# Performance work log

Measured on AMD Instinct MI355X. Metric: run time of the kernel, lower is better.

Reference implementation:

```python
import jax, jax.numpy as jnp
import numpy as np

DIM = 256
STATE = 128
RANK = 64
BATCH = 16
H = 64
W = 64
BLOCK = 64
LN_EPS = 1e-5


def _linear(z, w, b):
    # torch nn.Linear: z @ w.T + b, w: [out, in]
    return jnp.matmul(z, w.T) + b


def _depthwise_conv1d(y, conv_w, conv_b):
    # y: [B, L, D] -> torch Conv1d(D, D, k=7, pad=3, groups=D)
    lhs = jnp.transpose(y, (0, 2, 1))  # [B, D, L]
    out = jax.lax.conv_general_dilated(
        lhs, conv_w, window_strides=(1,), padding=[(3, 3)],
        feature_group_count=STATE,
        dimension_numbers=("NCH", "OIH", "NCH"))
    out = out + conv_b[None, :, None]
    return jnp.transpose(out, (0, 2, 1))  # [B, L, D]


def _scan_parallel(seq, in_proj_w, in_proj_b, U, V, B_w, B_b, out_w, out_b,
                   conv_w, conv_b):
    # seq: [B, L, C]; L > PARALLEL_THRESHOLD path of the torch module
    Bn, L, _ = seq.shape
    x = _linear(seq, in_proj_w, in_proj_b)   # [B, L, D]
    bx = _linear(x, B_w, B_b)                # [B, L, D]
    n_blocks = (L + BLOCK - 1) // BLOCK
    pad_len = n_blocks * BLOCK - L
    if pad_len > 0:
        bx = jnp.pad(bx, ((0, 0), (0, pad_len), (0, 0)))
    # [B, n_blocks, BLOCK, D] -> scan over time axis BLOCK
    bx_blocks = bx.reshape(Bn, n_blocks, BLOCK, STATE)
    bx_t = jnp.transpose(bx_blocks, (2, 0, 1, 3))  # [BLOCK, B, n_blocks, D]

    def step(h, xt):
        # h: [B, n_blocks, D]; low-rank transition h @ V @ U^T + Bx
        h = jnp.matmul(jnp.matmul(h, V), U.T) + xt
        return h, h

    h0 = jnp.zeros((Bn, n_blocks, STATE), dtype=seq.dtype)
    _, ys = jax.lax.scan(step, h0, bx_t)           # [BLOCK, B, n_blocks, D]
    y_flat = jnp.transpose(ys, (1, 2, 0, 3)).reshape(Bn, n_blocks * BLOCK, STATE)
    y_flat = y_flat + _depthwise_conv1d(y_flat, conv_w, conv_b)
    if pad_len > 0:
        y_flat = y_flat[:, :L, :]
    return _linear(y_flat, out_w, out_b)           # [B, L, C]


def _layer_norm(z, g, b):
    mu = jnp.mean(z, axis=-1, keepdims=True)
    var = jnp.var(z, axis=-1, keepdims=True)
    return (z - mu) * jax.lax.rsqrt(var + LN_EPS) * g + b


def setup_inputs() -> dict:
    key = jax.random.key(0)
    ks = jax.random.split(key, 16)
    s = 0.02
    return {
        "x": jax.random.normal(ks[0], (BATCH, DIM, H, W), dtype=jnp.float32),
        "in_proj_w": jax.random.normal(ks[1], (STATE, DIM)) * s,
        "in_proj_b": jnp.zeros((STATE,), jnp.float32),
        "U": jax.random.normal(ks[2], (STATE, RANK)) * s,
        "V": jax.random.normal(ks[3], (STATE, RANK)) * s,
        "B_w": jax.random.normal(ks[4], (STATE, STATE)) * s,
        "B_b": jnp.zeros((STATE,), jnp.float32),
        "out_w": jax.random.normal(ks[5], (DIM, STATE)) * s,
        "out_b": jnp.zeros((DIM,), jnp.float32),
        "gate_w": jax.random.normal(ks[6], (DIM, DIM)) * s,
        "gate_b": jnp.zeros((DIM,), jnp.float32),
        "norm_g": jnp.ones((DIM,), jnp.float32),
        "norm_b": jnp.zeros((DIM,), jnp.float32),
        "conv_w": jax.random.normal(ks[7], (STATE, 1, 7)) * s,
        "conv_b": jnp.zeros((STATE,), jnp.float32),
    }


def reference(x, in_proj_w, in_proj_b, U, V, B_w, B_b, out_w, out_b,
              gate_w, gate_b, norm_g, norm_b, conv_w, conv_b):
    Bn, C, h, w = x.shape
    seq_lr = jnp.transpose(x, (0, 2, 3, 1)).reshape(Bn, h * w, C)
    seq_rl = seq_lr[:, ::-1, :]
    scan = lambda s: _scan_parallel(s, in_proj_w, in_proj_b, U, V, B_w, B_b,
                                    out_w, out_b, conv_w, conv_b)
    y_lr = scan(seq_lr)
    y_rl = scan(seq_rl)[:, ::-1, :]
    y = 0.5 * (y_lr + y_rl)
    gate = jax.nn.sigmoid(_linear(seq_lr, gate_w, gate_b))
    y = gate * y
    y = _layer_norm(y + seq_lr, norm_g, norm_b)
    y = jnp.transpose(y.reshape(Bn, h, w, C), (0, 3, 1, 2))
    state_seq = _linear(seq_lr, in_proj_w, in_proj_b)
    return y, state_seq
```

## Files before the change

### kernel.cpp

```cpp
#include <hip/hip_runtime.h>
#include <hip/hip_bf16.h>

#define DIMC 256
#define STATE 128
#define RANK 64
#define NBATCH 16
#define LSEQ 4096
#define NROWS (NBATCH*LSEQ)
#define LN_EPS 1e-5f
#define XSTR 264
#define X1STR 136

typedef __attribute__((ext_vector_type(8))) short frag8;
typedef __attribute__((ext_vector_type(4))) float f32x4;

union Pack4 { __hip_bfloat16 h[4]; uint2 u; };
union Pack8 { __hip_bfloat16 h[8]; uint4 u; };

__device__ inline void gload_lds16(const void* g, void* l) {
    __builtin_amdgcn_global_load_lds((const __attribute__((address_space(1))) void*)g,
                                     (__attribute__((address_space(3))) void*)l, 16, 0, 0);
}

template<int NROWSW, int NTHR>
__device__ inline void stage_wslice(const __hip_bfloat16* __restrict__ W, int Krow, int k0,
                                    __hip_bfloat16* dst, int t) {
    constexpr int ROUNDS = (NROWSW*64) / (NTHR*16);
    const int lane = t & 63, w = t >> 6;
    #pragma unroll
    for (int j = 0; j < ROUNDS; ++j) {
        int base = (w*ROUNDS + j) << 10;
        int X = base + lane*16;
        int r = X >> 6;
        int cg = (X >> 4) & 3;
        const __hip_bfloat16* src = W + (size_t)r*Krow + k0 + ((cg ^ ((r>>1)&3)) << 3);
        gload_lds16(src, (char*)dst + base);
    }
}
__device__ inline frag8 ld_wfrag(const __hip_bfloat16* buf, int row, int q) {
    return *(const frag8*)((const char*)buf + (row<<6) + ((q ^ ((row>>1)&3))<<4));
}

__global__ __launch_bounds__(128) void a_kernel(const float* __restrict__ U, const float* __restrict__ V,
                                                __hip_bfloat16* __restrict__ At) {
    int i = blockIdx.x, j = threadIdx.x;
    float s = 0.f;
    #pragma unroll
    for (int r = 0; r < RANK; ++r) s += V[i*RANK + r] * U[j*RANK + r];
    At[j*STATE + i] = __float2bfloat16(s);
}

__global__ __launch_bounds__(256) void prep_weights(const float* __restrict__ in_w, const float* __restrict__ B_w,
                                                    const float* __restrict__ gate_w, const float* __restrict__ out_w,
                                                    __hip_bfloat16* __restrict__ in_wb, __hip_bfloat16* __restrict__ B_wb,
                                                    __hip_bfloat16* __restrict__ gate_wb, __hip_bfloat16* __restrict__ out_wb) {
    int idx = blockIdx.x*256 + threadIdx.x;
    int which = blockIdx.y;
    if (which == 0) { if (idx < STATE*DIMC)  in_wb[idx]   = __float2bfloat16(in_w[idx]); }
    else if (which == 1) { if (idx < STATE*STATE) B_wb[idx] = __float2bfloat16(B_w[idx]); }
    else if (which == 2) { if (idx < DIMC*DIMC)  gate_wb[idx] = __float2bfloat16(gate_w[idx]); }
    else { if (idx < DIMC*STATE) out_wb[idx] = __float2bfloat16(out_w[idx]); }
}

template<int NTHR>
__device__ inline void stage_x64(const float* __restrict__ xb, int l0,
                                 __hip_bfloat16* __restrict__ xs, int t) {
    constexpr int UN = 1024 / NTHR;
    #pragma unroll
    for (int uu = 0; uu < UN; ++uu) {
        int unit = t + uu*NTHR;
        int lg = unit & 15, cg = unit >> 4;
        int l = lg*4;
        float4 v0 = *(const float4*)(xb + (size_t)(cg*4+0)*LSEQ + l0 + l);
        float4 v1 = *(const float4*)(xb + (size_t)(cg*4+1)*LSEQ + l0 + l);
        float4 v2 = *(const float4*)(xb + (size_t)(cg*4+2)*LSEQ + l0 + l);
        float4 v3 = *(const float4*)(xb + (size_t)(cg*4+3)*LSEQ + l0 + l);
        const float* p0 = (const float*)&v0; const float* p1 = (const float*)&v1;
        const float* p2 = (const float*)&v2; const float* p3 = (const float*)&v3;
        #pragma unroll
        for (int li = 0; li < 4; ++li) {
            Pack4 p;
            p.h[0] = __float2bfloat16(p0[li]);
            p.h[1] = __float2bfloat16(p1[li]);
            p.h[2] = __float2bfloat16(p2[li]);
            p.h[3] = __float2bfloat16(p3[li]);
            int row = l + li;
            int col = (cg*4) ^ ((row&3)<<3);
            *(uint2*)(xs + (size_t)row*XSTR + col) = p.u;
        }
    }
}
__device__ inline frag8 ld_xfrag(const __hip_bfloat16* __restrict__ xs, int row, int k) {
    return *(const frag8*)(xs + (size_t)row*XSTR + (k ^ ((row&3)<<3)));
}

__global__ __launch_bounds__(512) void gemm_inB(const float* __restrict__ x,
                                                const __hip_bfloat16* __restrict__ in_wb, const float* __restrict__ in_b,
                                                const __hip_bfloat16* __restrict__ B_wb, const float* __restrict__ B_b,
                                                float* __restrict__ state_out, float* __restrict__ bx) {
    __shared__ __hip_bfloat16 xs[64*XSTR];
    __shared__ __hip_bfloat16 wsl[2][4096];
    __hip_bfloat16* x1s = xs;
    const int t = threadIdx.x;
    const int lane = t & 63;
    const int c = lane & 15, q = lane >> 4;
    const int w = t >> 6, wm = w >> 1, wc = w & 1;
    const int r0 = blockIdx.x * 64;
    const int b = r0 >> 12, l0 = r0 & 4095;

    stage_x64<512>(x + (size_t)b*DIMC*LSEQ, l0, xs, t);
    stage_wslice<STATE,512>(in_wb, DIMC, 0, wsl[0], t);
    __syncthreads();

    f32x4 acc[4] = {};
    #pragma unroll
    for (int i = 0; i < 8; ++i) {
        if (i < 7) stage_wslice<STATE,512>(in_wb, DIMC, (i+1)*32, wsl[(i+1)&1], t);
        frag8 af = ld_xfrag(xs, wm*16 + c, i*32 + q*8);
        #pragma unroll
        for (int nt = 0; nt < 4; ++nt) {
            frag8 bf = ld_wfrag(wsl[i&1], wc*64 + nt*16 + c, q);
            acc[nt] = __builtin_amdgcn_mfma_f32_16x16x32_bf16(af, bf, acc[nt], 0, 0, 0);
        }
        __syncthreads();
    }

    stage_wslice<STATE,512>(B_wb, STATE, 0, wsl[0], t);

    #pragma unroll
    for (int nt = 0; nt < 4; ++nt) {
        int col = wc*64 + nt*16 + c;
        float bb = in_b[col];
        #pragma unroll
        for (int r = 0; r < 4; ++r) {
            int row = wm*16 + q*4 + r;
            float v = acc[nt][r] + bb;
            state_out[(size_t)(r0 + row)*STATE + col] = v;
            x1s[(size_t)row*X1STR + (col ^ ((row&3)<<3))] = __float2bfloat16(v);
        }
    }
    __syncthreads();

    f32x4 acc2[4] = {};
    #pragma unroll
    for (int i = 0; i < 4; ++i) {
        if (i < 3) stage_wslice<STATE,512>(B_wb, STATE, (i+1)*32, wsl[(i+1)&1], t);
        int row = wm*16 + c;
        frag8 af = *(const frag8*)(x1s + (size_t)row*X1STR + (((i*32) + q*8) ^ ((row&3)<<3)));
        #pragma unroll
        for (int nt = 0; nt < 4; ++nt) {
            frag8 bf = ld_wfrag(wsl[i&1], wc*64 + nt*16 + c, q);
            acc2[nt] = __builtin_amdgcn_mfma_f32_16x16x32_bf16(af, bf, acc2[nt], 0, 0, 0);
        }
        __syncthreads();
    }
    const int orow = r0 + wm*16 + q*4;
    #pragma unroll
    for (int nt = 0; nt < 4; ++nt) {
        int col = wc*64 + nt*16 + c;
        float bb = B_b[col];
        #pragma unroll
        for (int r = 0; r < 4; ++r)
            bx[(size_t)(orow + r)*STATE + col] = acc2[nt][r] + bb;
    }
}

#define HSTRIDE 144
__global__ __launch_bounds__(256, 1) void scan_mfma(const float* __restrict__ bx,
                                                    const __hip_bfloat16* __restrict__ At,
                                                    __hip_bfloat16* __restrict__ ylr,
                                                    __hip_bfloat16* __restrict__ yrl) {
    __shared__ __hip_bfloat16 Hb[16 * HSTRIDE];
    const int t = threadIdx.x;
    const int l = t & 63;
    const int wm = t >> 6;
    const int c = l & 15;
    const int q = l >> 4;

    const int S   = blockIdx.x * 16 + c;
    const int dir = S >> 10;
    const int b   = (S >> 6) & 15;
    const int blk = S & 63;
    const int lp0 = blk * 64;
    const int lorig0 = dir ? (LSEQ - 1 - lp0) : lp0;
    const int sgnstep = dir ? -STATE : STATE;

    const float* bxrow = bx + ((size_t)b*LSEQ + lorig0)*STATE;
    __hip_bfloat16* yrow = (dir ? yrl : ylr) + ((size_t)b*LSEQ + lp0)*STATE;

    frag8 afr[2][4];
    #pragma unroll
    for (int mm = 0; mm < 2; ++mm)
        #pragma unroll
        for (int kc = 0; kc < 4; ++kc)
            afr[mm][kc] = *(const frag8*)(At + (size_t)((wm*2+mm)*16 + c)*STATE + kc*32 + q*8);

    for (int k = t; k < 16*HSTRIDE; k += 256) Hb[k] = __float2bfloat16(0.f);
    __syncthreads();

    f32x4 pf[2];
    #pragma unroll
    for (int mm = 0; mm < 2; ++mm)
        pf[mm] = *(const f32x4*)(bxrow + (wm*2+mm)*16 + q*4);

    for (int tt = 0; tt < 64; ++tt) {
        frag8 bfr[4];
        #pragma unroll
        for (int kc = 0; kc < 4; ++kc)
            bfr[kc] = *(const frag8*)(&Hb[c*HSTRIDE + kc*32 + q*8]);

        f32x4 acc[2];
        #pragma unroll
        for (int mm = 0; mm < 2; ++mm) {
            f32x4 a = {0.f, 0.f, 0.f, 0.f};
            #pragma unroll
            for (int kc = 0; kc < 4; ++kc)
                a = __builtin_amdgcn_mfma_f32_16x16x32_bf16(afr[mm][kc], bfr[kc], a, 0, 0, 0);
            acc[mm] = a + pf[mm];
        }
        if (tt < 63) {
            bxrow += sgnstep;
            #pragma unroll
            for (int mm = 0; mm < 2; ++mm)
                pf[mm] = *(const f32x4*)(bxrow + (wm*2+mm)*16 + q*4);
        }

        Pack4 pk[2];
        #pragma unroll
        for (int mm = 0; mm < 2; ++mm) {
            pk[mm].h[0] = __float2bfloat16(acc[mm][0]);
            pk[mm].h[1] = __float2bfloat16(acc[mm][1]);
            pk[mm].h[2] = __float2bfloat16(acc[mm][2]);
            pk[mm].h[3] = __float2bfloat16(acc[mm][3]);
        }
        #pragma unroll
        for (int mm = 0; mm < 2; ++mm)
            *(uint2*)(yrow + (wm*2+mm)*16 + q*4) = pk[mm].u;
        yrow += STATE;

        __syncthreads();
        #pragma unroll
        for (int mm = 0; mm < 2; ++mm)
            *(uint2*)(&Hb[c*HSTRIDE + (wm*2+mm)*16 + q*4]) = pk[mm].u;
        __syncthreads();
    }
}

__global__ __launch_bounds__(128) void conv_combine(const __hip_bfloat16* __restrict__ ylr,
                                                    const __hip_bfloat16* __restrict__ yrl,
                                                    const float* __restrict__ conv_w, const float* __restrict__ conv_b,
                                                    __hip_bfloat16* __restrict__ u) {
    const int t = threadIdx.x;
    const int s8 = (t & 15) * 8;
    const int l = blockIdx.x * 8 + (t >> 4);
    const int b = blockIdx.y;

    float wv[8][7];
    #pragma unroll
    for (int j = 0; j < 8; ++j)
        #pragma unroll
        for (int i = 0; i < 7; ++i) wv[j][i] = conv_w[(s8+j)*7 + i];

    const __hip_bfloat16* plr = ylr + (size_t)b*LSEQ*STATE;
    const __hip_bfloat16* prl = yrl + (size_t)b*LSEQ*STATE;

    float acc[8];
    {
        Pack8 v; v.u = *(const uint4*)(plr + (size_t)l*STATE + s8);
        #pragma unroll
        for (int j = 0; j < 8; ++j) acc[j] = __bfloat162float(v.h[j]);
    }
    #pragma unroll
    for (int i = 0; i < 7; ++i) {
        int qq = l - 3 + i;
        if (qq >= 0 && qq < LSEQ) {
            Pack8 v; v.u = *(const uint4*)(plr + (size_t)qq*STATE + s8);
            #pragma unroll
            for (int j = 0; j < 8; ++j) acc[j] += wv[j][i] * __bfloat162float(v.h[j]);
        }
    }
    const int lp = LSEQ - 1 - l;
    {
        Pack8 v; v.u = *(const uint4*)(prl + (size_t)lp*STATE + s8);
        #pragma unroll
        for (int j = 0; j < 8; ++j) acc[j] += __bfloat162float(v.h[j]);
    }
    #pragma unroll
    for (int i = 0; i < 7; ++i) {
        int qq = lp - 3 + i;
        if (qq >= 0 && qq < LSEQ) {
            Pack8 v; v.u = *(const uint4*)(prl + (size_t)qq*STATE + s8);
            #pragma unroll
            for (int j = 0; j < 8; ++j) acc[j] += wv[j][i] * __bfloat162float(v.h[j]);
        }
    }
    Pack8 o;
    #pragma unroll
    for (int j = 0; j < 8; ++j) o.h[j] = __float2bfloat16(0.5f*acc[j] + conv_b[s8+j]);
    *(uint4*)(u + ((size_t)b*LSEQ + l)*STATE + s8) = o.u;
}

__global__ __launch_bounds__(512) void fused_out(const float* __restrict__ x, const __hip_bfloat16* __restrict__ ub,
    const __hip_bfloat16* __restrict__ out_wb, const float* __restrict__ out_b,
    const __hip_bfloat16* __restrict__ gate_wb, const float* __restrict__ gate_b,
    const float* __restrict__ norm_g, const float* __restrict__ norm_b,
    float* __restrict__ y) {
    __shared__ __hip_bfloat16 xs[64*XSTR];
    __shared__ __hip_bfloat16 wsl[2][8192];
    __shared__ float lnbuf[4][2][16][2];
    const int t = threadIdx.x;
    const int lane = t & 63, c = lane & 15, q = lane >> 4;
    const int w = t >> 6, wm = w >> 1, wc = w & 1;
    const int r0 = blockIdx.x * 64;
    const int b = r0 >> 12, l0 = r0 & 4095;

    stage_x64<512>(x + (size_t)b*DIMC*LSEQ, l0, xs, t);
    frag8 ufr[4];
    {
        const int arow = r0 + wm*16 + c;
        #pragma unroll
        for (int kc = 0; kc < 4; ++kc)
            ufr[kc] = *(const frag8*)(ub + (size_t)arow*STATE + kc*32 + q*8);
    }
    stage_wslice<DIMC,512>(gate_wb, DIMC, 0, wsl[0], t);
    __syncthreads();

    f32x4 accg[8] = {};
    f32x4 acco[8] = {};
    #pragma unroll
    for (int i = 0; i < 12; ++i) {
        if (i < 11) {
            if (i < 7) stage_wslice<DIMC,512>(gate_wb, DIMC, (i+1)*32, wsl[(i+1)&1], t);
            else       stage_wslice<DIMC,512>(out_wb,  STATE, (i-7)*32, wsl[(i+1)&1], t);
        }
        if (i < 8) {
            frag8 af = ld_xfrag(xs, wm*16 + c, i*32 + q*8);
            #pragma unroll
            for (int nt = 0; nt < 8; ++nt) {
                frag8 bf = ld_wfrag(wsl[i&1], wc*128 + nt*16 + c, q);
                accg[nt] = __builtin_amdgcn_mfma_f32_16x16x32_bf16(af, bf, accg[nt], 0, 0, 0);
            }
        } else {
            frag8 af = ufr[i-8];
            #pragma unroll
            for (int nt = 0; nt < 8; ++nt) {
                frag8 bf = ld_wfrag(wsl[i&1], wc*128 + nt*16 + c, q);
                acco[nt] = __builtin_amdgcn_mfma_f32_16x16x32_bf16(af, bf, acco[nt], 0, 0, 0);
            }
        }
        __syncthreads();
    }

    float s1[4] = {0.f,0.f,0.f,0.f}, s2[4] = {0.f,0.f,0.f,0.f};
    #pragma unroll
    for (int nt = 0; nt < 8; ++nt) {
        int col = wc*128 + nt*16 + c;
        float gb = gate_b[col], ob = out_b[col];
        #pragma unroll
        for (int r = 0; r < 4; ++r) {
            int row = wm*16 + q*4 + r;
            float res = __bfloat162float(xs[(size_t)row*XSTR + (col ^ ((row&3)<<3))]);
            float g = 1.f/(1.f + expf(-(accg[nt][r] + gb)));
            float v = g*(acco[nt][r] + ob) + res;
            accg[nt][r] = v;
            s1[r] += v; s2[r] += v*v;
        }
    }
    #pragma unroll
    for (int m = 1; m <= 8; m <<= 1) {
        #pragma unroll
        for (int r = 0; r < 4; ++r) {
            s1[r] += __shfl_xor(s1[r], m);
            s2[r] += __shfl_xor(s2[r], m);
        }
    }
    if (c == 0) {
        #pragma unroll
        for (int r = 0; r < 4; ++r) {
            lnbuf[wm][wc][q*4 + r][0] = s1[r];
            lnbuf[wm][wc][q*4 + r][1] = s2[r];
        }
    }
    __syncthreads();
    float mu[4], rstd[4];
    #pragma unroll
    for (int r = 0; r < 4; ++r) {
        int row16 = q*4 + r;
        float t1 = lnbuf[wm][0][row16][0] + lnbuf[wm][1][row16][0];
        float t2 = lnbuf[wm][0][row16][1] + lnbuf[wm][1][row16][1];
        float m_ = t1 * (1.f/256.f);
        mu[r] = m_;
        rstd[r] = rsqrtf(t2 * (1.f/256.f) - m_*m_ + LN_EPS);
    }
    #pragma unroll
    for (int nt = 0; nt < 8; ++nt) {
        int col = wc*128 + nt*16 + c;
        float g = norm_g[col], be = norm_b[col];
        float4 v4;
        v4.x = (accg[nt][0] - mu[0]) * rstd[0] * g + be;
        v4.y = (accg[nt][1] - mu[1]) * rstd[1] * g + be;
        v4.z = (accg[nt][2] - mu[2]) * rstd[2] * g + be;
        v4.w = (accg[nt][3] - mu[3]) * rstd[3] * g + be;
        *(float4*)(y + ((size_t)b*DIMC + col)*LSEQ + l0 + wm*16 + q*4) = v4;
    }
}

extern "C" void kernel_launch(void* const* d_in, const int* in_sizes, int n_in,
                              void* d_out, int out_size, void* d_ws, size_t ws_size,
                              hipStream_t stream) {
    const float* x      = (const float*)d_in[0];
    const float* in_w   = (const float*)d_in[1];
    const float* in_b   = (const float*)d_in[2];
    const float* U      = (const float*)d_in[3];
    const float* V      = (const float*)d_in[4];
    const float* B_w    = (const float*)d_in[5];
    const float* B_b    = (const float*)d_in[6];
    const float* out_w  = (const float*)d_in[7];
    const float* out_b  = (const float*)d_in[8];
    const float* gate_w = (const float*)d_in[9];
    const float* gate_b = (const float*)d_in[10];
    const float* norm_g = (const float*)d_in[11];
    const float* norm_b = (const float*)d_in[12];
    const float* conv_w = (const float*)d_in[13];
    const float* conv_b = (const float*)d_in[14];

    float* yfinal = (float*)d_out;
    float* state_out = yfinal + (size_t)NBATCH*DIMC*LSEQ;

    float* ws  = (float*)d_ws;
    float* bxu = ws;
    __hip_bfloat16* ub = (__hip_bfloat16*)ws;
    __hip_bfloat16* Atb16  = (__hip_bfloat16*)(ws + (size_t)NROWS*STATE);
    __hip_bfloat16* in_wb  = Atb16 + STATE*STATE;
    __hip_bfloat16* B_wb   = in_wb + STATE*DIMC;
    __hip_bfloat16* gate_wb= B_wb + STATE*STATE;
    __hip_bfloat16* out_wb = gate_wb + DIMC*DIMC;

    __hip_bfloat16* ylr = (__hip_bfloat16*)yfinal;
    __hip_bfloat16* yrl = ylr + (size_t)NROWS*STATE;

    a_kernel<<<dim3(STATE), dim3(STATE), 0, stream>>>(U, V, Atb16);
    prep_weights<<<dim3(256, 4), dim3(256), 0, stream>>>(in_w, B_w, gate_w, out_w,
                                                         in_wb, B_wb, gate_wb, out_wb);
    gemm_inB<<<dim3(NROWS/64), dim3(512), 0, stream>>>(x, in_wb, in_b, B_wb, B_b, state_out, bxu);
    scan_mfma<<<dim3(128), dim3(256), 0, stream>>>(bxu, Atb16, ylr, yrl);
    conv_combine<<<dim3(LSEQ/8, NBATCH), dim3(128), 0, stream>>>(ylr, yrl, conv_w, conv_b, ub);
    fused_out<<<dim3(NROWS/64), dim3(512), 0, stream>>>(x, ub, out_wb, out_b, gate_wb, gate_b,
                                                        norm_g, norm_b, yfinal);
    (void)in_sizes; (void)n_in; (void)out_size; (void)ws_size;
}
```

Measured before the change: 150.8 us.

## Store bx in bf16 and pipeline weight staging with explicit waitcnt barriers

The intermediate bx tensor is now written in bf16 instead of fp32, which halves its write traffic in gemm_inB and its read traffic in the serial scan kernel. The __syncthreads calls in the GEMM loops are replaced with manual s_waitcnt vmcnt/lgkmcnt plus s_barrier sequences, so the async LDS loads for the next weight slice stay in flight across the barrier. The B_w slice prefetch is folded into the last in_proj iteration, and the state_out store is deferred to the end. The risks are lower bx precision feeding the recurrence and correctness depending on hand-tuned vmcnt counts.

Result: slower. 168.8 us (+12.0%).

```diff
diff --git a/kernel.cpp b/kernel.cpp
--- a/kernel.cpp
+++ b/kernel.cpp
@@ -10,6 +10,10 @@
 #define LN_EPS 1e-5f
 #define XSTR 264
 #define X1STR 136
+
+#define SBAR() asm volatile("s_barrier" ::: "memory")
+#define SCHED_FENCE() __builtin_amdgcn_sched_barrier(0)
+#define LGKM0() asm volatile("s_waitcnt lgkmcnt(0)" ::: "memory")
 
 typedef __attribute__((ext_vector_type(8))) short frag8;
 typedef __attribute__((ext_vector_type(4))) float f32x4;
@@ -97,7 +101,7 @@
 __global__ __launch_bounds__(512) void gemm_inB(const float* __restrict__ x,
                                                 const __hip_bfloat16* __restrict__ in_wb, const float* __restrict__ in_b,
                                                 const __hip_bfloat16* __restrict__ B_wb, const float* __restrict__ B_b,
-                                                float* __restrict__ state_out, float* __restrict__ bx) {
+                                                float* __restrict__ state_out, __hip_bfloat16* __restrict__ bxb) {
     __shared__ __hip_bfloat16 xs[64*XSTR];
     __shared__ __hip_bfloat16 wsl[2][4096];
     __hip_bfloat16* x1s = xs;
@@ -115,18 +119,27 @@
     f32x4 acc[4] = {};
     #pragma unroll
     for (int i = 0; i < 8; ++i) {
-        if (i < 7) stage_wslice<STATE,512>(in_wb, DIMC, (i+1)*32, wsl[(i+1)&1], t);
+        LGKM0();
+        SCHED_FENCE();
+        SBAR();
+        if (i < 7) {
+            stage_wslice<STATE,512>(in_wb, DIMC, (i+1)*32, wsl[(i+1)&1], t);
+        } else {
+            stage_wslice<STATE,512>(B_wb, STATE, 0, wsl[0], t);
+        }
+        asm volatile("s_waitcnt vmcnt(1)" ::: "memory");
+        SBAR();
         frag8 af = ld_xfrag(xs, wm*16 + c, i*32 + q*8);
         #pragma unroll
         for (int nt = 0; nt < 4; ++nt) {
             frag8 bf = ld_wfrag(wsl[i&1], wc*64 + nt*16 + c, q);
             acc[nt] = __builtin_amdgcn_mfma_f32_16x16x32_bf16(af, bf, acc[nt], 0, 0, 0);
         }
-        __syncthreads();
-    }
-
-    stage_wslice<STATE,512>(B_wb, STATE, 0, wsl[0], t);
-
+    }
+
+    LGKM0();
+    SCHED_FENCE();
+    SBAR();
     #pragma unroll
     for (int nt = 0; nt < 4; ++nt) {
         int col = wc*64 + nt*16 + c;
@@ -134,17 +147,26 @@
         #pragma unroll
         for (int r = 0; r < 4; ++r) {
             int row = wm*16 + q*4 + r;
-            float v = acc[nt][r] + bb;
-            state_out[(size_t)(r0 + row)*STATE + col] = v;
-            x1s[(size_t)row*X1STR + (col ^ ((row&3)<<3))] = __float2bfloat16(v);
-        }
-    }
-    __syncthreads();
+            x1s[(size_t)row*X1STR + (col ^ ((row&3)<<3))] = __float2bfloat16(acc[nt][r] + bb);
+        }
+    }
+    LGKM0();
+    SCHED_FENCE();
+    SBAR();
 
     f32x4 acc2[4] = {};
     #pragma unroll
     for (int i = 0; i < 4; ++i) {
-        if (i < 3) stage_wslice<STATE,512>(B_wb, STATE, (i+1)*32, wsl[(i+1)&1], t);
+        LGKM0();
+        SCHED_FENCE();
+        SBAR();
+        if (i < 3) {
+            stage_wslice<STATE,512>(B_wb, STATE, (i+1)*32, wsl[(i+1)&1], t);
+            asm volatile("s_waitcnt vmcnt(1)" ::: "memory");
+        } else {
+            asm volatile("s_waitcnt vmcnt(0)" ::: "memory");
+        }
+        SBAR();
         int row = wm*16 + c;
         frag8 af = *(const frag8*)(x1s + (size_t)row*X1STR + (((i*32) + q*8) ^ ((row&3)<<3)));
         #pragma unroll
@@ -152,21 +174,23 @@
             frag8 bf = ld_wfrag(wsl[i&1], wc*64 + nt*16 + c, q);
             acc2[nt] = __builtin_amdgcn_mfma_f32_16x16x32_bf16(af, bf, acc2[nt], 0, 0, 0);
         }
-        __syncthreads();
-    }
+    }
+
     const int orow = r0 + wm*16 + q*4;
     #pragma unroll
     for (int nt = 0; nt < 4; ++nt) {
         int col = wc*64 + nt*16 + c;
-        float bb = B_b[col];
-        #pragma unroll
-        for (int r = 0; r < 4; ++r)
-            bx[(size_t)(orow + r)*STATE + col] = acc2[nt][r] + bb;
+        float bi = in_b[col], bb = B_b[col];
+        #pragma unroll
+        for (int r = 0; r < 4; ++r) {
+            state_out[(size_t)(orow + r)*STATE + col] = acc[nt][r] + bi;
+            bxb[(size_t)(orow + r)*STATE + col] = __float2bfloat16(acc2[nt][r] + bb);
+        }
     }
 }
 
 #define HSTRIDE 144
-__global__ __launch_bounds__(256, 1) void scan_mfma(const float* __restrict__ bx,
+__global__ __launch_bounds__(256, 1) void scan_mfma(const __hip_bfloat16* __restrict__ bxb,
                                                     const __hip_bfloat16* __restrict__ At,
                                                     __hip_bfloat16* __restrict__ ylr,
                                                     __hip_bfloat16* __restrict__ yrl) {
@@ -185,7 +209,7 @@
     const int lorig0 = dir ? (LSEQ - 1 - lp0) : lp0;
     const int sgnstep = dir ? -STATE : STATE;
 
-    const float* bxrow = bx + ((size_t)b*LSEQ + lorig0)*STATE;
+    const __hip_bfloat16* bxrow = bxb + ((size_t)b*LSEQ + lorig0)*STATE;
     __hip_bfloat16* yrow = (dir ? yrl : ylr) + ((size_t)b*LSEQ + lp0)*STATE;
 
     frag8 afr[2][4];
@@ -198,10 +222,10 @@
     for (int k = t; k < 16*HSTRIDE; k += 256) Hb[k] = __float2bfloat16(0.f);
     __syncthreads();
 
-    f32x4 pf[2];
+    uint2 pf[2];
     #pragma unroll
     for (int mm = 0; mm < 2; ++mm)
-        pf[mm] = *(const f32x4*)(bxrow + (wm*2+mm)*16 + q*4);
+        pf[mm] = *(const uint2*)(bxrow + (wm*2+mm)*16 + q*4);
 
     for (int tt = 0; tt < 64; ++tt) {
         frag8 bfr[4];
@@ -216,13 +240,17 @@
             #pragma unroll
             for (int kc = 0; kc < 4; ++kc)
                 a = __builtin_amdgcn_mfma_f32_16x16x32_bf16(afr[mm][kc], bfr[kc], a, 0, 0, 0);
-            acc[mm] = a + pf[mm];
+            Pack4 pp; pp.u = pf[mm];
+            acc[mm][0] = a[0] + __bfloat162float(pp.h[0]);
+            acc[mm][1] = a[1] + __bfloat162float(pp.h[1]);
+            acc[mm][2] = a[2] + __bfloat162float(pp.h[2]);
+            acc[mm][3] = a[3] + __bfloat162float(pp.h[3]);
         }
         if (tt < 63) {
             bxrow += sgnstep;
             #pragma unroll
             for (int mm = 0; mm < 2; ++mm)
-                pf[mm] = *(const f32x4*)(bxrow + (wm*2+mm)*16 + q*4);
+                pf[mm] = *(const uint2*)(bxrow + (wm*2+mm)*16 + q*4);
         }
 
         Pack4 pk[2];
@@ -329,10 +357,17 @@
     f32x4 acco[8] = {};
     #pragma unroll
     for (int i = 0; i < 12; ++i) {
+        LGKM0();
+        SCHED_FENCE();
+        SBAR();
         if (i < 11) {
             if (i < 7) stage_wslice<DIMC,512>(gate_wb, DIMC, (i+1)*32, wsl[(i+1)&1], t);
             else       stage_wslice<DIMC,512>(out_wb,  STATE, (i-7)*32, wsl[(i+1)&1], t);
-        }
+            asm volatile("s_waitcnt vmcnt(2)" ::: "memory");
+        } else {
+            asm volatile("s_waitcnt vmcnt(0)" ::: "memory");
+        }
+        SBAR();
         if (i < 8) {
             frag8 af = ld_xfrag(xs, wm*16 + c, i*32 + q*8);
             #pragma unroll
@@ -348,8 +383,10 @@
                 acco[nt] = __builtin_amdgcn_mfma_f32_16x16x32_bf16(af, bf, acco[nt], 0, 0, 0);
             }
         }
-        __syncthreads();
-    }
+    }
+    LGKM0();
+    SCHED_FENCE();
+    __syncthreads();
 
     float s1[4] = {0.f,0.f,0.f,0.f}, s2[4] = {0.f,0.f,0.f,0.f};
     #pragma unroll
@@ -428,8 +465,8 @@
     float* state_out = yfinal + (size_t)NBATCH*DIMC*LSEQ;
 
     float* ws  = (float*)d_ws;
-    float* bxu = ws;
-    __hip_bfloat16* ub = (__hip_bfloat16*)ws;
+    __hip_bfloat16* bxb = (__hip_bfloat16*)ws;
+    __hip_bfloat16* ub  = (__hip_bfloat16*)ws;
     __hip_bfloat16* Atb16  = (__hip_bfloat16*)(ws + (size_t)NROWS*STATE);
     __hip_bfloat16* in_wb  = Atb16 + STATE*STATE;
     __hip_bfloat16* B_wb   = in_wb + STATE*DIMC;
@@ -442,8 +479,8 @@
     a_kernel<<<dim3(STATE), dim3(STATE), 0, stream>>>(U, V, Atb16);
     prep_weights<<<dim3(256, 4), dim3(256), 0, stream>>>(in_w, B_w, gate_w, out_w,
                                                          in_wb, B_wb, gate_wb, out_wb);
-    gemm_inB<<<dim3(NROWS/64), dim3(512), 0, stream>>>(x, in_wb, in_b, B_wb, B_b, state_out, bxu);
-    scan_mfma<<<dim3(128), dim3(256), 0, stream>>>(bxu, Atb16, ylr, yrl);
+    gemm_inB<<<dim3(NROWS/64), dim3(512), 0, stream>>>(x, in_wb, in_b, B_wb, B_b, state_out, bxb);
+    scan_mfma<<<dim3(128), dim3(256), 0, stream>>>(bxb, Atb16, ylr, yrl);
     conv_combine<<<dim3(LSEQ/8, NBATCH), dim3(128), 0, stream>>>(ylr, yrl, conv_w, conv_b, ub);
     fused_out<<<dim3(NROWS/64), dim3(512), 0, stream>>>(x, ub, out_wb, out_b, gate_wb, gate_b,
                                                         norm_g, norm_b, yfinal);
```

## Store bx in bf16 and reuse transposed bf16 x in output kernel

Applied to the files above, without the earlier changes.

gemm_inB now writes the transposed, bf16-converted x tile to a workspace buffer. fused_out loads that buffer straight into LDS with global_load_lds instead of re-reading and transposing the fp32 NCHW input. The bx intermediate is also stored as bf16 instead of fp32, which halves scan input traffic. The LDS swizzle widens from row&3 to row&7. The aim is less global memory traffic, at the cost of an extra bf16 x write, bf16 rounding of bx before the recurrence, and reliance on the workspace having room for x_bt.

After: 170.4 us. 13.0% more time.

```diff
diff --git a/kernel.cpp b/kernel.cpp
--- a/kernel.cpp
+++ b/kernel.cpp
@@ -85,19 +85,23 @@
             p.h[2] = __float2bfloat16(p2[li]);
             p.h[3] = __float2bfloat16(p3[li]);
             int row = l + li;
-            int col = (cg*4) ^ ((row&3)<<3);
+            int col = (cg*4) ^ ((row&7)<<3);
             *(uint2*)(xs + (size_t)row*XSTR + col) = p.u;
         }
     }
 }
 __device__ inline frag8 ld_xfrag(const __hip_bfloat16* __restrict__ xs, int row, int k) {
-    return *(const frag8*)(xs + (size_t)row*XSTR + (k ^ ((row&3)<<3)));
+    return *(const frag8*)(xs + (size_t)row*XSTR + (k ^ ((row&7)<<3)));
+}
+__device__ inline frag8 ld_xfrag2(const __hip_bfloat16* __restrict__ xs, int row, int k) {
+    return *(const frag8*)(xs + (size_t)row*DIMC + (k ^ ((row&7)<<3)));
 }
 
 __global__ __launch_bounds__(512) void gemm_inB(const float* __restrict__ x,
                                                 const __hip_bfloat16* __restrict__ in_wb, const float* __restrict__ in_b,
                                                 const __hip_bfloat16* __restrict__ B_wb, const float* __restrict__ B_b,
-                                                float* __restrict__ state_out, float* __restrict__ bx) {
+                                                float* __restrict__ state_out, __hip_bfloat16* __restrict__ bxb,
+                                                __hip_bfloat16* __restrict__ x_bt) {
     __shared__ __hip_bfloat16 xs[64*XSTR];
     __shared__ __hip_bfloat16 wsl[2][4096];
     __hip_bfloat16* x1s = xs;
@@ -112,6 +116,15 @@
     stage_wslice<STATE,512>(in_wb, DIMC, 0, wsl[0], t);
     __syncthreads();
 
+    {
+        int row = t >> 3, sub = t & 7;
+        const char* srcb = (const char*)xs + (size_t)row*(XSTR*2) + sub*64;
+        __hip_bfloat16* dstp = x_bt + (size_t)(r0 + row)*DIMC + sub*32;
+        #pragma unroll
+        for (int j = 0; j < 4; ++j)
+            *(uint4*)(dstp + j*8) = *(const uint4*)(srcb + j*16);
+    }
+
     f32x4 acc[4] = {};
     #pragma unroll
     for (int i = 0; i < 8; ++i) {
@@ -161,12 +174,12 @@
         float bb = B_b[col];
         #pragma unroll
         for (int r = 0; r < 4; ++r)
-            bx[(size_t)(orow + r)*STATE + col] = acc2[nt][r] + bb;
+            bxb[(size_t)(orow + r)*STATE + col] = __float2bfloat16(acc2[nt][r] + bb);
     }
 }
 
 #define HSTRIDE 144
-__global__ __launch_bounds__(256, 1) void scan_mfma(const float* __restrict__ bx,
+__global__ __launch_bounds__(256, 1) void scan_mfma(const __hip_bfloat16* __restrict__ bxb,
                                                     const __hip_bfloat16* __restrict__ At,
                                                     __hip_bfloat16* __restrict__ ylr,
                                                     __hip_bfloat16* __restrict__ yrl) {
@@ -185,7 +198,7 @@
     const int lorig0 = dir ? (LSEQ - 1 - lp0) : lp0;
     const int sgnstep = dir ? -STATE : STATE;
 
-    const float* bxrow = bx + ((size_t)b*LSEQ + lorig0)*STATE;
+    const __hip_bfloat16* bxrow = bxb + ((size_t)b*LSEQ + lorig0)*STATE;
     __hip_bfloat16* yrow = (dir ? yrl : ylr) + ((size_t)b*LSEQ + lp0)*STATE;
 
     frag8 afr[2][4];
@@ -198,10 +211,10 @@
     for (int k = t; k < 16*HSTRIDE; k += 256) Hb[k] = __float2bfloat16(0.f);
     __syncthreads();
 
-    f32x4 pf[2];
+    uint2 pf[2];
     #pragma unroll
     for (int mm = 0; mm < 2; ++mm)
-        pf[mm] = *(const f32x4*)(bxrow + (wm*2+mm)*16 + q*4);
+        pf[mm] = *(const uint2*)(bxrow + (wm*2+mm)*16 + q*4);
 
     for (int tt = 0; tt < 64; ++tt) {
         frag8 bfr[4];
@@ -216,13 +229,17 @@
             #pragma unroll
             for (int kc = 0; kc < 4; ++kc)
                 a = __builtin_amdgcn_mfma_f32_16x16x32_bf16(afr[mm][kc], bfr[kc], a, 0, 0, 0);
-            acc[mm] = a + pf[mm];
+            Pack4 pp; pp.u = pf[mm];
+            acc[mm][0] = a[0] + __bfloat162float(pp.h[0]);
+            acc[mm][1] = a[1] + __bfloat162float(pp.h[1]);
+            acc[mm][2] = a[2] + __bfloat162float(pp.h[2]);
+            acc[mm][3] = a[3] + __bfloat162float(pp.h[3]);
         }
         if (tt < 63) {
             bxrow += sgnstep;
             #pragma unroll
             for (int mm = 0; mm < 2; ++mm)
-                pf[mm] = *(const f32x4*)(bxrow + (wm*2+mm)*16 + q*4);
+                pf[mm] = *(const uint2*)(bxrow + (wm*2+mm)*16 + q*4);
         }
 
         Pack4 pk[2];
@@ -300,12 +317,13 @@
     *(uint4*)(u + ((size_t)b*LSEQ + l)*STATE + s8) = o.u;
 }
 
-__global__ __launch_bounds__(512) void fused_out(const float* __restrict__ x, const __hip_bfloat16* __restrict__ ub,
+__global__ __launch_bounds__(512) void fused_out(const __hip_bfloat16* __restrict__ x_bt,
+    const __hip_bfloat16* __restrict__ ub,
     const __hip_bfloat16* __restrict__ out_wb, const float* __restrict__ out_b,
     const __hip_bfloat16* __restrict__ gate_wb, const float* __restrict__ gate_b,
     const float* __restrict__ norm_g, const float* __restrict__ norm_b,
     float* __restrict__ y) {
-    __shared__ __hip_bfloat16 xs[64*XSTR];
+    __shared__ __hip_bfloat16 xs2[64*DIMC];
     __shared__ __hip_bfloat16 wsl[2][8192];
     __shared__ float lnbuf[4][2][16][2];
     const int t = threadIdx.x;
@@ -314,7 +332,14 @@
     const int r0 = blockIdx.x * 64;
     const int b = r0 >> 12, l0 = r0 & 4095;
 
-    stage_x64<512>(x + (size_t)b*DIMC*LSEQ, l0, xs, t);
+    {
+        const char* srcx = (const char*)(x_bt + (size_t)r0*DIMC);
+        #pragma unroll
+        for (int j = 0; j < 4; ++j) {
+            int base = (w*256 + j*64) * 16;
+            gload_lds16(srcx + base + lane*16, (char*)xs2 + base);
+        }
+    }
     frag8 ufr[4];
     {
         const int arow = r0 + wm*16 + c;
@@ -334,7 +359,7 @@
             else       stage_wslice<DIMC,512>(out_wb,  STATE, (i-7)*32, wsl[(i+1)&1], t);
         }
         if (i < 8) {
-            frag8 af = ld_xfrag(xs, wm*16 + c, i*32 + q*8);
+            frag8 af = ld_xfrag2(xs2, wm*16 + c, i*32 + q*8);
             #pragma unroll
             for (int nt = 0; nt < 8; ++nt) {
                 frag8 bf = ld_wfrag(wsl[i&1], wc*128 + nt*16 + c, q);
@@ -359,7 +384,7 @@
         #pragma unroll
         for (int r = 0; r < 4; ++r) {
             int row = wm*16 + q*4 + r;
-            float res = __bfloat162float(xs[(size_t)row*XSTR + (col ^ ((row&3)<<3))]);
+            float res = __bfloat162float(xs2[(size_t)row*DIMC + (col ^ ((row&7)<<3))]);
             float g = 1.f/(1.f + expf(-(accg[nt][r] + gb)));
             float v = g*(acco[nt][r] + ob) + res;
             accg[nt][r] = v;
@@ -428,13 +453,14 @@
     float* state_out = yfinal + (size_t)NBATCH*DIMC*LSEQ;
 
     float* ws  = (float*)d_ws;
-    float* bxu = ws;
-    __hip_bfloat16* ub = (__hip_bfloat16*)ws;
+    __hip_bfloat16* bxb = (__hip_bfloat16*)ws;
+    __hip_bfloat16* ub  = (__hip_bfloat16*)ws;
     __hip_bfloat16* Atb16  = (__hip_bfloat16*)(ws + (size_t)NROWS*STATE);
     __hip_bfloat16* in_wb  = Atb16 + STATE*STATE;
     __hip_bfloat16* B_wb   = in_wb + STATE*DIMC;
     __hip_bfloat16* gate_wb= B_wb + STATE*STATE;
     __hip_bfloat16* out_wb = gate_wb + DIMC*DIMC;
+    __hip_bfloat16* x_bt   = out_wb + DIMC*STATE;
 
     __hip_bfloat16* ylr = (__hip_bfloat16*)yfinal;
     __hip_bfloat16* yrl = ylr + (size_t)NROWS*STATE;
@@ -442,10 +468,11 @@
     a_kernel<<<dim3(STATE), dim3(STATE), 0, stream>>>(U, V, Atb16);
     prep_weights<<<dim3(256, 4), dim3(256), 0, stream>>>(in_w, B_w, gate_w, out_w,
                                                          in_wb, B_wb, gate_wb, out_wb);
-    gemm_inB<<<dim3(NROWS/64), dim3(512), 0, stream>>>(x, in_wb, in_b, B_wb, B_b, state_out, bxu);
-    scan_mfma<<<dim3(128), dim3(256), 0, stream>>>(bxu, Atb16, ylr, yrl);
+    gemm_inB<<<dim3(NROWS/64), dim3(512), 0, stream>>>(x, in_wb, in_b, B_wb, B_b,
+                                                       state_out, bxb, x_bt);
+    scan_mfma<<<dim3(128), dim3(256), 0, stream>>>(bxb, Atb16, ylr, yrl);
     conv_combine<<<dim3(LSEQ/8, NBATCH), dim3(128), 0, stream>>>(ylr, yrl, conv_w, conv_b, ub);
-    fused_out<<<dim3(NROWS/64), dim3(512), 0, stream>>>(x, ub, out_wb, out_b, gate_wb, gate_b,
+    fused_out<<<dim3(NROWS/64), dim3(512), 0, stream>>>(x_bt, ub, out_wb, out_b, gate_wb, gate_b,
                                                         norm_g, norm_b, yfinal);
     (void)in_sizes; (void)n_in; (void)out_size; (void)ws_size;
 }
```
